# Kernel tuning notes

Measured on AMD Instinct MI355X. Metric: run time of the kernel, lower is better.

Reference implementation:

```python
import jax, jax.numpy as jnp
import numpy as np

N, G, D, H, B = 32768, 1024, 512, 768, 4   # nodes, graphs, hidden, shared, branches
GHD, NHD = 64, 3                           # graph head dim, node head dim (var_output=1)

def setup_inputs() -> dict:
    key = jax.random.key(0)
    ks = jax.random.split(key, 8)
    scale = 0.02
    x = jax.random.normal(ks[0], (N, D), dtype=jnp.float32)
    batch = jnp.sort(jax.random.randint(ks[1], (N,), 0, G, dtype=jnp.int32))
    dataset_name = jax.random.randint(ks[2], (G,), 0, B, dtype=jnp.int32)
    return {
        "x": x,
        "batch": batch,
        "dataset_name": dataset_name,
        "Wg_shared": jax.random.normal(ks[3], (B, D, H), jnp.float32) * scale,
        "bg_shared": jnp.zeros((B, H), jnp.float32),
        "Wg_head": jax.random.normal(ks[4], (B, H, 2 * GHD), jnp.float32) * scale,
        "bg_head": jnp.zeros((B, 2 * GHD), jnp.float32),
        "Wn1": jax.random.normal(ks[5], (B, D, D), jnp.float32) * scale,
        "bn1": jnp.zeros((B, D), jnp.float32),
        "Wn2": jax.random.normal(ks[6], (B, D, 2 * NHD), jnp.float32) * scale,
        "bn2": jnp.zeros((B, 2 * NHD), jnp.float32),
    }

def _select_branch(y, branch_ids):
    # y: [n, B, f], branch_ids: [n] -> [n, f]
    return jnp.take_along_axis(y, branch_ids[:, None, None], axis=1)[:, 0]

def reference(x, batch, dataset_name, Wg_shared, bg_shared, Wg_head, bg_head,
              Wn1, bn1, Wn2, bn2):
    nG = dataset_name.shape[0]
    # --- graph mean pooling (graph_pool_fn with reduction='mean') ---
    counts = jax.ops.segment_sum(jnp.ones((x.shape[0], 1), x.dtype), batch,
                                 num_segments=nG)
    x_graph = jax.ops.segment_sum(x, batch, num_segments=nG) / jnp.maximum(counts, 1.0)
    # --- graph head: per-dataset-ID branch dispatch (dense-MoE form) ---
    hg = jax.nn.relu(jnp.einsum('gd,bdh->gbh', x_graph, Wg_shared) + bg_shared)  # [G,B,H]
    hg_sel = _select_branch(hg, dataset_name)                                    # [G,H]
    og = jnp.einsum('gh,bho->gbo', hg_sel, Wg_head) + bg_head                    # [G,B,2*GHD]
    og_sel = _select_branch(og, dataset_name)
    graph_head = og_sel[:, :GHD]
    graph_var = og_sel[:, GHD:] ** 2
    # --- node head: route nodes by their graph's dataset ID (repeat_interleave) ---
    node_branch = dataset_name[batch]                                            # [N]
    hn = jax.nn.relu(jnp.einsum('nd,bdh->nbh', x, Wn1) + bn1)                    # [N,B,D]
    hn_sel = _select_branch(hn, node_branch)                                     # [N,D]
    on = jnp.einsum('nh,bho->nbo', hn_sel, Wn2) + bn2                            # [N,B,2*NHD]
    on_sel = _select_branch(on, node_branch)
    node_head = on_sel[:, :NHD]
    node_var = on_sel[:, NHD:] ** 2
    # torch returns (outputs, outputs_var); flattened here as 4 arrays
    return (graph_head, node_head, graph_var, node_var)
```

## Files before the change

### kernel.cpp

```cpp
#include <hip/hip_runtime.h>

#define N_NODES 32768
#define G_GRAPHS 1024
#define D_DIM 512
#define H_DIM 768
#define B_BR 4
#define GHD 64
#define NHD 3

#define NH_OFF (G_GRAPHS * GHD)
#define GV_OFF (G_GRAPHS * GHD + N_NODES * NHD)
#define NV_OFF (2 * G_GRAPHS * GHD + N_NODES * NHD)

typedef unsigned short ushort_t;
typedef __attribute__((ext_vector_type(8))) short short8;
typedef __attribute__((ext_vector_type(4))) float f32x4;
typedef __attribute__((ext_vector_type(4))) ushort_t ushort4_t;

__device__ __forceinline__ ushort_t rne_bf16(float v) {
  unsigned bits = __float_as_uint(v);
  return (ushort_t)((bits + 0x7fffu + ((bits >> 16) & 1u)) >> 16);
}

__global__ __launch_bounds__(1024) void segscan_kernel(
    const int* __restrict__ batch, const int* __restrict__ dsname,
    int* __restrict__ gstart, int* __restrict__ goff, int* __restrict__ glist,
    int* __restrict__ cnt, int* __restrict__ gcnt, int* __restrict__ pbase) {
  __shared__ int sg[G_GRAPHS + 1];
  __shared__ int scnt[4], sgcnt[4];
  const int tid = threadIdx.x;
  {
    int g = tid;
    int lo = 0, hi = N_NODES;
    while (lo < hi) { int mid = (lo + hi) >> 1; if (batch[mid] < g) lo = mid + 1; else hi = mid; }
    sg[g] = lo; gstart[g] = lo;
    if (tid == 0) { sg[G_GRAPHS] = N_NODES; gstart[G_GRAPHS] = N_NODES; }
  }
  __syncthreads();
  if (tid < 256) {
    const int lane = tid & 63;
    const int b = tid >> 6;
    int run_n = 0, run_g = 0;
    for (int c = 0; c < G_GRAPHS / 64; ++c) {
      int g = c * 64 + lane;
      int mine = (dsname[g] == b) ? 1 : 0;
      int len = mine ? (sg[g + 1] - sg[g]) : 0;
      int sl = len, so = mine;
#pragma unroll
      for (int off = 1; off < 64; off <<= 1) {
        int tl = __shfl_up(sl, off);
        int to = __shfl_up(so, off);
        if (lane >= off) { sl += tl; so += to; }
      }
      if (mine) {
        goff[g] = run_n + sl - len;
        glist[b * G_GRAPHS + run_g + so - 1] = g;
      }
      run_n += __shfl(sl, 63);
      run_g += __shfl(so, 63);
    }
    if (lane == 0) { scnt[b] = run_n; sgcnt[b] = run_g; }
  }
  __syncthreads();
  if (tid == 0) {
    int p = 0;
    for (int b2 = 0; b2 < 4; ++b2) {
      cnt[b2] = scnt[b2];
      gcnt[b2] = sgcnt[b2];
      pbase[b2] = p;
      p += (scnt[b2] + 63) & ~63;
    }
  }
}

__global__ __launch_bounds__(256) void prep_kernel(
    const float* __restrict__ x, const int* __restrict__ batch,
    const int* __restrict__ dsname, const int* __restrict__ gstart,
    const int* __restrict__ goff, const int* __restrict__ pbase,
    int* __restrict__ lists, ushort_t* __restrict__ xp,
    ushort_t* __restrict__ xgb,
    const float* __restrict__ Wn1, ushort_t* __restrict__ WPh,
    const float* __restrict__ Wg1, ushort_t* __restrict__ WG1,
    const float* __restrict__ Wgh, ushort_t* __restrict__ WG2,
    const float* __restrict__ Wn2, ushort_t* __restrict__ W2T) {
  __shared__ float Ws[64][65];
  const int bid = blockIdx.x;
  const int tid = threadIdx.x;

  if (bid < 512) {
    const int rl = tid >> 6;
    const int cs = tid & 63;
    float* red = (float*)Ws;
#pragma unroll
    for (int gi = 0; gi < 2; ++gi) {
      int g = bid * 2 + gi;
      int start = gstart[g], end = gstart[g + 1];
      int len = end - start;
      int b = dsname[g];
      int og = goff[g];
      int off0 = pbase[b] + og;
      float s0 = 0.f, s1 = 0.f, s2 = 0.f, s3 = 0.f;
      float s4 = 0.f, s5 = 0.f, s6 = 0.f, s7 = 0.f;
      for (int i = rl; i < len; i += 4) {
        int n = start + i;
        const float* sp = x + (size_t)n * D_DIM + cs * 8;
        float4 v0 = *reinterpret_cast<const float4*>(sp);
        float4 v1 = *reinterpret_cast<const float4*>(sp + 4);
        s0 += v0.x; s1 += v0.y; s2 += v0.z; s3 += v0.w;
        s4 += v1.x; s5 += v1.y; s6 += v1.z; s7 += v1.w;
        short8 h;
        h[0] = (short)rne_bf16(v0.x); h[1] = (short)rne_bf16(v0.y);
        h[2] = (short)rne_bf16(v0.z); h[3] = (short)rne_bf16(v0.w);
        h[4] = (short)rne_bf16(v1.x); h[5] = (short)rne_bf16(v1.y);
        h[6] = (short)rne_bf16(v1.z); h[7] = (short)rne_bf16(v1.w);
        int ib = og + i;
        *reinterpret_cast<short8*>(xp + (size_t)(off0 + i) * 512 + (cs ^ (ib & 7)) * 8) = h;
        if (cs == 0) lists[b * N_NODES + ib] = n;
      }
      float* rr = red + (rl * 64 + cs) * 8;
      rr[0] = s0; rr[1] = s1; rr[2] = s2; rr[3] = s3;
      rr[4] = s4; rr[5] = s5; rr[6] = s6; rr[7] = s7;
      __syncthreads();
      if (rl == 0) {
        float inv = (len > 0) ? 1.0f / (float)len : 0.0f;
        short8 h;
#pragma unroll
        for (int k = 0; k < 8; ++k) {
          float tot = red[(0 * 64 + cs) * 8 + k] + red[(1 * 64 + cs) * 8 + k] +
                      red[(2 * 64 + cs) * 8 + k] + red[(3 * 64 + cs) * 8 + k];
          h[k] = (short)rne_bf16(tot * inv);
        }
        *reinterpret_cast<short8*>(xgb + (size_t)g * D_DIM + cs * 8) = h;
      }
      __syncthreads();
    }
  } else {
    const int cid = bid - 512;
    if (cid < 256) {
      int b = cid >> 6, t = cid & 63;
      int kt = t >> 3, nt = t & 7;
      const float* W = Wn1 + (size_t)b * D_DIM * D_DIM;
      for (int i = tid; i < 64 * 64; i += 256) {
        int k = i >> 6, n = i & 63;
        Ws[k][n] = W[(size_t)(kt * 64 + k) * D_DIM + nt * 64 + n];
      }
      __syncthreads();
      for (int i = tid; i < 64 * 8; i += 256) {
        int n = i >> 3, kq8 = i & 7;
        short8 sh;
#pragma unroll
        for (int j = 0; j < 8; ++j) sh[j] = (short)rne_bf16(Ws[kq8 * 8 + j][n]);
        int gn = nt * 64 + n, gk0 = kt * 64 + kq8 * 8;
        int n16 = gn >> 4, l15 = gn & 15;
        int ks = gk0 >> 5, lq = (gk0 >> 3) & 3;
        size_t off = ((((size_t)b * 32 + n16) * 16 + ks) * 64 + lq * 16 + l15) * 8;
        *reinterpret_cast<short8*>(WPh + off) = sh;
      }
    } else if (cid < 640) {
      int l2 = cid - 256;
      int b = l2 / 96, t = l2 % 96;
      int kt = t / 12, nt = t % 12;
      const float* W = Wg1 + (size_t)b * D_DIM * H_DIM;
      for (int i = tid; i < 64 * 64; i += 256) {
        int k = i >> 6, n = i & 63;
        Ws[k][n] = W[(size_t)(kt * 64 + k) * H_DIM + nt * 64 + n];
      }
      __syncthreads();
      for (int i = tid; i < 64 * 8; i += 256) {
        int n = i >> 3, kq8 = i & 7;
        short8 sh;
#pragma unroll
        for (int j = 0; j < 8; ++j) sh[j] = (short)rne_bf16(Ws[kq8 * 8 + j][n]);
        int gn = nt * 64 + n, gk0 = kt * 64 + kq8 * 8;
        int n16 = gn >> 4, l15 = gn & 15;
        int ks = gk0 >> 5, lq = (gk0 >> 3) & 3;
        size_t off = ((((size_t)b * 48 + n16) * 16 + ks) * 64 + lq * 16 + l15) * 8;
        *reinterpret_cast<short8*>(WG1 + off) = sh;
      }
    } else if (cid < 644) {
      int b = cid - 640;
      const float* W = Wgh + (size_t)b * H_DIM * 2 * GHD;
      for (int i = tid; i < 8 * 24 * 64; i += 256) {
        int n16 = i / (24 * 64);
        int rem = i % (24 * 64);
        int ks = rem / 64, lane = rem % 64;
        int l15 = lane & 15, lq = lane >> 4;
        int o = n16 * 16 + l15;
        short8 sv;
#pragma unroll
        for (int j = 0; j < 8; ++j) {
          int k = ks * 32 + lq * 8 + j;
          sv[j] = (short)rne_bf16(W[(size_t)k * 128 + o]);
        }
        *reinterpret_cast<short8*>(WG2 + (size_t)i * 8 + (size_t)b * (8 * 24 * 64 * 8)) = sv;
      }
    } else {
      int b = cid - 644;
      for (int i = tid; i < 16 * D_DIM; i += 256) {
        int o = i & 15, c = i >> 4;
        float v = (o < 6) ? Wn2[(size_t)b * D_DIM * 6 + c * 6 + o] : 0.0f;
        W2T[(size_t)b * 16 * D_DIM + o * D_DIM + c] = rne_bf16(v);
      }
    }
  }
}

#define NBM 64
#define GRAPH_BLOCKS 128
#define NODE_BLOCKS 576

__global__ __launch_bounds__(512, 2) void mega_kernel(
    const ushort_t* __restrict__ xpacked,
    const ushort_t* __restrict__ WPh,
    const float* __restrict__ bn1,
    const ushort_t* __restrict__ W2T, const float* __restrict__ bn2,
    const int* __restrict__ cnt, const int* __restrict__ pbase,
    const int* __restrict__ lists,
    const ushort_t* __restrict__ xgb,
    const ushort_t* __restrict__ WG1, const float* __restrict__ bg_shared,
    const ushort_t* __restrict__ WG2, const float* __restrict__ bg_head,
    const int* __restrict__ gcnt, const int* __restrict__ glist,
    float* __restrict__ out) {
  __shared__ __align__(16) char smem[131072];
  __shared__ int idxbuf[64];

  const int bid = blockIdx.x;
  const int tid = threadIdx.x;
  const int lane = tid & 63;
  const int w = tid >> 6;
  const int l15 = lane & 15;
  const int lq = lane >> 4;

  if (bid >= GRAPH_BLOCKS) {
    const int nb = bid - GRAPH_BLOCKS;
    const int b = (nb & 7) >> 1;
    const int tile = ((nb >> 3) << 1) | (nb & 1);
    const int count = cnt[b];
    const int base = tile * NBM;
    if (base >= count) return;
    const int tile_base = pbase[b] + base;

    ushort_t* Ah = (ushort_t*)smem;
    if (tid < NBM) {
      int r = base + tid;
      idxbuf[tid] = (r < count) ? lists[b * N_NODES + r] : lists[b * N_NODES];
    }

    const char* srow = (const char*)(xpacked + (size_t)tile_base * 512);
#pragma unroll
    for (int i = 0; i < 8; ++i) {
      int row = w * 8 + i;
      const void* gsrc = srow + (size_t)row * 1024 + (size_t)lane * 16;
      __builtin_amdgcn_global_load_lds(
          (const __attribute__((address_space(1))) void*)gsrc,
          (__attribute__((address_space(3))) void*)((char*)Ah + row * 1024),
          16, 0, 0);
    }
    __syncthreads();

    const ushort_t* __restrict__ wph =
        WPh + (((size_t)b * 32 + w * 4) * 16) * 512 + (size_t)lane * 8;
    ushort_t* Bl = (ushort_t*)(smem + 65536 + w * 8192);

#pragma unroll
    for (int ct = 0; ct < 4; ++ct) {
      __builtin_amdgcn_global_load_lds(
          (const __attribute__((address_space(1))) void*)(wph + (size_t)(ct * 16) * 512),
          (__attribute__((address_space(3))) void*)(Bl + ct * 512),
          16, 0, 0);
    }

    f32x4 acc[4][4];
#pragma unroll
    for (int i = 0; i < 4; ++i)
#pragma unroll
      for (int j = 0; j < 4; ++j) acc[i][j] = (f32x4){0.f, 0.f, 0.f, 0.f};

#pragma unroll
    for (int ks = 0; ks < 16; ++ks) {
      const int nks = (ks + 1) & 15;
      ushort_t* Bnx = Bl + ((ks + 1) & 1) * 2048;
#pragma unroll
      for (int ct = 0; ct < 4; ++ct) {
        __builtin_amdgcn_global_load_lds(
            (const __attribute__((address_space(1))) void*)(wph + (size_t)(ct * 16 + nks) * 512),
            (__attribute__((address_space(3))) void*)(Bnx + ct * 512),
            16, 0, 0);
      }
      asm volatile("s_waitcnt vmcnt(4)" ::: "memory");
      __builtin_amdgcn_sched_barrier(0);
      const ushort_t* Bc = Bl + (ks & 1) * 2048;
      short8 ah[4], bh[4];
#pragma unroll
      for (int rt = 0; rt < 4; ++rt) {
        int R = rt * 16 + l15;
        int byteoff = R * 1024 + ((ks * 64 + lq * 16) ^ ((R & 7) << 4));
        ah[rt] = *reinterpret_cast<const short8*>((const char*)Ah + byteoff);
      }
#pragma unroll
      for (int ct = 0; ct < 4; ++ct)
        bh[ct] = *reinterpret_cast<const short8*>(Bc + ct * 512 + lane * 8);
#pragma unroll
      for (int ct = 0; ct < 4; ++ct) {
#pragma unroll
        for (int rt = 0; rt < 4; ++rt) {
          acc[rt][ct] = __builtin_amdgcn_mfma_f32_16x16x32_bf16(ah[rt], bh[ct], acc[rt][ct], 0, 0, 0);
        }
      }
    }

    __syncthreads();
    ushort_t* hn = Ah;
#pragma unroll
    for (int ct = 0; ct < 4; ++ct) {
      int n = w * 64 + ct * 16 + l15;
      float bias = bn1[b * D_DIM + n];
#pragma unroll
      for (int rt = 0; rt < 4; ++rt) {
#pragma unroll
        for (int j = 0; j < 4; ++j) {
          int row = rt * 16 + lq * 4 + j;
          float v = fmaxf(acc[rt][ct][j] + bias, 0.0f);
          int byteoff = row * 1024 + ((n * 2) ^ ((row & 7) << 4));
          *reinterpret_cast<ushort_t*>((char*)hn + byteoff) = rne_bf16(v);
        }
      }
    }
    __syncthreads();

    if (w < 4) {
      f32x4 acc2 = (f32x4){0.f, 0.f, 0.f, 0.f};
      const ushort_t* __restrict__ w2 =
          W2T + (size_t)b * (16 * 512) + (size_t)l15 * 512 + lq * 8;
      const int R = w * 16 + l15;
#pragma unroll
      for (int ks = 0; ks < 16; ++ks) {
        int byteoff = R * 1024 + ((ks * 64 + lq * 16) ^ ((R & 7) << 4));
        short8 a2 = *reinterpret_cast<const short8*>((const char*)hn + byteoff);
        short8 b2 = *reinterpret_cast<const short8*>(w2 + ks * 32);
        acc2 = __builtin_amdgcn_mfma_f32_16x16x32_bf16(a2, b2, acc2, 0, 0, 0);
      }
      int o = l15;
      if (o < 6) {
        float bo = bn2[b * 6 + o];
#pragma unroll
        for (int j = 0; j < 4; ++j) {
          int r = w * 16 + lq * 4 + j;
          if (base + r < count) {
            int n = idxbuf[r];
            float v = acc2[j] + bo;
            if (o < NHD) out[NH_OFF + n * NHD + o] = v;
            else out[NV_OFF + n * NHD + (o - NHD)] = v * v;
          }
        }
      }
    }
  } else {
    const int gb = bid;
    const int b = (gb & 7) >> 1;
    const int tile = ((gb >> 3) << 1) | (gb & 1);
    const int gc = gcnt[b];
    const int base = tile * 32;
    if (base >= gc) return;

    ushort_t* Ag = (ushort_t*)smem;
    if (tid < 32) {
      int r = base + tid;
      idxbuf[tid] = (r < gc) ? glist[b * G_GRAPHS + r] : glist[b * G_GRAPHS];
    }
    __syncthreads();

#pragma unroll
    for (int it = 0; it < 4; ++it) {
      int u = it * 512 + tid;
      int r = u >> 6, cp = u & 63;
      const ushort_t* sp = xgb + (size_t)idxbuf[r] * D_DIM + cp * 8;
      short8 h = *reinterpret_cast<const short8*>(sp);
      int byteoff = r * 1024 + ((cp * 16) ^ ((r & 7) << 4));
      *reinterpret_cast<short8*>((char*)Ag + byteoff) = h;
    }
    __syncthreads();

    f32x4 acc[2][6];
#pragma unroll
    for (int i = 0; i < 2; ++i)
#pragma unroll
      for (int j = 0; j < 6; ++j) acc[i][j] = (f32x4){0.f, 0.f, 0.f, 0.f};

    const ushort_t* __restrict__ g1 =
        WG1 + (((size_t)b * 48 + w * 6) * 16) * 512 + (size_t)lane * 8;

    for (int ks = 0; ks < 16; ++ks) {
      short8 ah[2];
#pragma unroll
      for (int rt = 0; rt < 2; ++rt) {
        int R = rt * 16 + l15;
        int byteoff = R * 1024 + ((ks * 64 + lq * 16) ^ ((R & 7) << 4));
        ah[rt] = *reinterpret_cast<const short8*>((const char*)Ag + byteoff);
      }
#pragma unroll
      for (int ct = 0; ct < 6; ++ct) {
        short8 bh = *reinterpret_cast<const short8*>(g1 + (size_t)(ct * 16 + ks) * 512);
#pragma unroll
        for (int rt = 0; rt < 2; ++rt) {
          acc[rt][ct] = __builtin_amdgcn_mfma_f32_16x16x32_bf16(ah[rt], bh, acc[rt][ct], 0, 0, 0);
        }
      }
    }

    __syncthreads();
    ushort_t* hgs = (ushort_t*)smem;
#pragma unroll
    for (int ct = 0; ct < 6; ++ct) {
      int n = w * 96 + ct * 16 + l15;
      float bias = bg_shared[b * H_DIM + n];
#pragma unroll
      for (int rt = 0; rt < 2; ++rt) {
#pragma unroll
        for (int j = 0; j < 4; ++j) {
          int row = rt * 16 + lq * 4 + j;
          float v = fmaxf(acc[rt][ct][j] + bias, 0.0f);
          int byteoff = row * 1536 + ((n * 2) ^ ((row & 7) << 4));
          *reinterpret_cast<ushort_t*>((char*)hgs + byteoff) = rne_bf16(v);
        }
      }
    }
    __syncthreads();

    f32x4 acc2[2];
    acc2[0] = (f32x4){0.f, 0.f, 0.f, 0.f};
    acc2[1] = (f32x4){0.f, 0.f, 0.f, 0.f};
    const ushort_t* __restrict__ g2 =
        WG2 + ((size_t)(b * 8 + w) * 24 * 64 + lane) * 8;

    for (int ks = 0; ks < 24; ++ks) {
      short8 b2 = *reinterpret_cast<const short8*>(g2 + (size_t)ks * 512);
#pragma unroll
      for (int rt = 0; rt < 2; ++rt) {
        int R = rt * 16 + l15;
        int byteoff = R * 1536 + ((ks * 64 + lq * 16) ^ ((R & 7) << 4));
        short8 a2 = *reinterpret_cast<const short8*>((const char*)hgs + byteoff);
        acc2[rt] = __builtin_amdgcn_mfma_f32_16x16x32_bf16(a2, b2, acc2[rt], 0, 0, 0);
      }
    }

    int o = w * 16 + l15;
    float bo = bg_head[b * 2 * GHD + o];
#pragma unroll
    for (int rt = 0; rt < 2; ++rt) {
#pragma unroll
      for (int j = 0; j < 4; ++j) {
        int r = rt * 16 + lq * 4 + j;
        if (base + r < gc) {
          int g = idxbuf[r];
          float v = acc2[rt][j] + bo;
          if (o < GHD) out[g * GHD + o] = v;
          else out[GV_OFF + g * GHD + (o - GHD)] = v * v;
        }
      }
    }
  }
}

extern "C" void kernel_launch(void* const* d_in, const int* in_sizes, int n_in,
                              void* d_out, int out_size, void* d_ws, size_t ws_size,
                              hipStream_t stream) {
  const float* x         = (const float*)d_in[0];
  const int*   batch     = (const int*)d_in[1];
  const int*   dsname    = (const int*)d_in[2];
  const float* Wg_shared = (const float*)d_in[3];
  const float* bg_shared = (const float*)d_in[4];
  const float* Wg_head   = (const float*)d_in[5];
  const float* bg_head   = (const float*)d_in[6];
  const float* Wn1       = (const float*)d_in[7];
  const float* bn1       = (const float*)d_in[8];
  const float* Wn2       = (const float*)d_in[9];
  const float* bn2       = (const float*)d_in[10];
  float* out = (float*)d_out;

  int* ws_i   = (int*)d_ws;
  int* cnt    = ws_i;
  int* gcnt   = ws_i + 8;
  int* pbase  = ws_i + 12;
  int* gstart = ws_i + 16;
  int* goff   = ws_i + 1056;
  int* glist  = ws_i + 2080;
  int* lists  = ws_i + 6176;
  ushort_t* xgb  = (ushort_t*)(ws_i + 137248);
  ushort_t* WPh  = xgb + 524288;
  ushort_t* W2T  = WPh + 1048576;
  ushort_t* WG1  = W2T + 32768;
  ushort_t* WG2  = WG1 + 1572864;
  ushort_t* xpacked = WG2 + 393216;

  segscan_kernel<<<1, 1024, 0, stream>>>(batch, dsname, gstart, goff, glist,
                                         cnt, gcnt, pbase);
  prep_kernel<<<1160, 256, 0, stream>>>(x, batch, dsname, gstart, goff, pbase,
                                        lists, xpacked, xgb,
                                        Wn1, WPh, Wg_shared, WG1,
                                        Wg_head, WG2, Wn2, W2T);
  mega_kernel<<<GRAPH_BLOCKS + NODE_BLOCKS, 512, 0, stream>>>(
      xpacked, WPh, bn1, W2T, bn2, cnt, pbase, lists,
      xgb, WG1, bg_shared, WG2, bg_head, gcnt, glist, out);
}
```

Before: 87.79 us.

## Widen prep parallelism, vectorize weight loads, reorder mega blocks and LDS waits

Result: slower. 94.10 us (+7.2%).

```diff
diff --git a/kernel.cpp b/kernel.cpp
--- a/kernel.cpp
+++ b/kernel.cpp
@@ -87,62 +87,71 @@
   const int bid = blockIdx.x;
   const int tid = threadIdx.x;
 
-  if (bid < 512) {
+  if (bid < 1024) {
     const int rl = tid >> 6;
     const int cs = tid & 63;
+    const int g = bid;
+    const int start = gstart[g];
+    const int len = gstart[g + 1] - start;
+    const int b = dsname[g];
+    const int og = goff[g];
+    const size_t off0 = (size_t)pbase[b] + og;
+    float s[8] = {0.f, 0.f, 0.f, 0.f, 0.f, 0.f, 0.f, 0.f};
+    for (int i0 = rl * 4; i0 < len; i0 += 16) {
+      float4 va[4], vb[4];
+#pragma unroll
+      for (int u = 0; u < 4; ++u) {
+        int i = i0 + u;
+        if (i < len) {
+          const float* sp = x + (size_t)(start + i) * D_DIM + cs * 8;
+          va[u] = *reinterpret_cast<const float4*>(sp);
+          vb[u] = *reinterpret_cast<const float4*>(sp + 4);
+        }
+      }
+#pragma unroll
+      for (int u = 0; u < 4; ++u) {
+        int i = i0 + u;
+        if (i < len) {
+          s[0] += va[u].x; s[1] += va[u].y; s[2] += va[u].z; s[3] += va[u].w;
+          s[4] += vb[u].x; s[5] += vb[u].y; s[6] += vb[u].z; s[7] += vb[u].w;
+          short8 h;
+          h[0] = (short)rne_bf16(va[u].x); h[1] = (short)rne_bf16(va[u].y);
+          h[2] = (short)rne_bf16(va[u].z); h[3] = (short)rne_bf16(va[u].w);
+          h[4] = (short)rne_bf16(vb[u].x); h[5] = (short)rne_bf16(vb[u].y);
+          h[6] = (short)rne_bf16(vb[u].z); h[7] = (short)rne_bf16(vb[u].w);
+          int ib = og + i;
+          *reinterpret_cast<short8*>(xp + (off0 + i) * 512 + (cs ^ (ib & 7)) * 8) = h;
+          if (cs == 0) lists[b * N_NODES + ib] = start + i;
+        }
+      }
+    }
     float* red = (float*)Ws;
-#pragma unroll
-    for (int gi = 0; gi < 2; ++gi) {
-      int g = bid * 2 + gi;
-      int start = gstart[g], end = gstart[g + 1];
-      int len = end - start;
-      int b = dsname[g];
-      int og = goff[g];
-      int off0 = pbase[b] + og;
-      float s0 = 0.f, s1 = 0.f, s2 = 0.f, s3 = 0.f;
-      float s4 = 0.f, s5 = 0.f, s6 = 0.f, s7 = 0.f;
-      for (int i = rl; i < len; i += 4) {
-        int n = start + i;
-        const float* sp = x + (size_t)n * D_DIM + cs * 8;
-        float4 v0 = *reinterpret_cast<const float4*>(sp);
-        float4 v1 = *reinterpret_cast<const float4*>(sp + 4);
-        s0 += v0.x; s1 += v0.y; s2 += v0.z; s3 += v0.w;
-        s4 += v1.x; s5 += v1.y; s6 += v1.z; s7 += v1.w;
-        short8 h;
-        h[0] = (short)rne_bf16(v0.x); h[1] = (short)rne_bf16(v0.y);
-        h[2] = (short)rne_bf16(v0.z); h[3] = (short)rne_bf16(v0.w);
-        h[4] = (short)rne_bf16(v1.x); h[5] = (short)rne_bf16(v1.y);
-        h[6] = (short)rne_bf16(v1.z); h[7] = (short)rne_bf16(v1.w);
-        int ib = og + i;
-        *reinterpret_cast<short8*>(xp + (size_t)(off0 + i) * 512 + (cs ^ (ib & 7)) * 8) = h;
-        if (cs == 0) lists[b * N_NODES + ib] = n;
-      }
-      float* rr = red + (rl * 64 + cs) * 8;
-      rr[0] = s0; rr[1] = s1; rr[2] = s2; rr[3] = s3;
-      rr[4] = s4; rr[5] = s5; rr[6] = s6; rr[7] = s7;
-      __syncthreads();
-      if (rl == 0) {
-        float inv = (len > 0) ? 1.0f / (float)len : 0.0f;
-        short8 h;
-#pragma unroll
-        for (int k = 0; k < 8; ++k) {
-          float tot = red[(0 * 64 + cs) * 8 + k] + red[(1 * 64 + cs) * 8 + k] +
-                      red[(2 * 64 + cs) * 8 + k] + red[(3 * 64 + cs) * 8 + k];
-          h[k] = (short)rne_bf16(tot * inv);
-        }
-        *reinterpret_cast<short8*>(xgb + (size_t)g * D_DIM + cs * 8) = h;
-      }
-      __syncthreads();
+    float* rr = red + (rl * 64 + cs) * 8;
+#pragma unroll
+    for (int k = 0; k < 8; ++k) rr[k] = s[k];
+    __syncthreads();
+    if (rl == 0) {
+      float inv = (len > 0) ? 1.0f / (float)len : 0.0f;
+      short8 h;
+#pragma unroll
+      for (int k = 0; k < 8; ++k) {
+        float tot = red[(0 * 64 + cs) * 8 + k] + red[(1 * 64 + cs) * 8 + k] +
+                    red[(2 * 64 + cs) * 8 + k] + red[(3 * 64 + cs) * 8 + k];
+        h[k] = (short)rne_bf16(tot * inv);
+      }
+      *reinterpret_cast<short8*>(xgb + (size_t)g * D_DIM + cs * 8) = h;
     }
   } else {
-    const int cid = bid - 512;
+    const int cid = bid - 1024;
     if (cid < 256) {
       int b = cid >> 6, t = cid & 63;
       int kt = t >> 3, nt = t & 7;
       const float* W = Wn1 + (size_t)b * D_DIM * D_DIM;
-      for (int i = tid; i < 64 * 64; i += 256) {
-        int k = i >> 6, n = i & 63;
-        Ws[k][n] = W[(size_t)(kt * 64 + k) * D_DIM + nt * 64 + n];
+      for (int i = tid; i < 64 * 16; i += 256) {
+        int k = i >> 4, n4 = (i & 15) << 2;
+        float4 v = *reinterpret_cast<const float4*>(
+            &W[(size_t)(kt * 64 + k) * D_DIM + nt * 64 + n4]);
+        Ws[k][n4] = v.x; Ws[k][n4 + 1] = v.y; Ws[k][n4 + 2] = v.z; Ws[k][n4 + 3] = v.w;
       }
       __syncthreads();
       for (int i = tid; i < 64 * 8; i += 256) {
@@ -161,9 +170,11 @@
       int b = l2 / 96, t = l2 % 96;
       int kt = t / 12, nt = t % 12;
       const float* W = Wg1 + (size_t)b * D_DIM * H_DIM;
-      for (int i = tid; i < 64 * 64; i += 256) {
-        int k = i >> 6, n = i & 63;
-        Ws[k][n] = W[(size_t)(kt * 64 + k) * H_DIM + nt * 64 + n];
+      for (int i = tid; i < 64 * 16; i += 256) {
+        int k = i >> 4, n4 = (i & 15) << 2;
+        float4 v = *reinterpret_cast<const float4*>(
+            &W[(size_t)(kt * 64 + k) * H_DIM + nt * 64 + n4]);
+        Ws[k][n4] = v.x; Ws[k][n4 + 1] = v.y; Ws[k][n4 + 2] = v.z; Ws[k][n4 + 3] = v.w;
       }
       __syncthreads();
       for (int i = tid; i < 64 * 8; i += 256) {
@@ -206,8 +217,8 @@
 }
 
 #define NBM 64
+#define NODE_BLOCKS 576
 #define GRAPH_BLOCKS 128
-#define NODE_BLOCKS 576
 
 __global__ __launch_bounds__(512, 2) void mega_kernel(
     const ushort_t* __restrict__ xpacked,
@@ -231,8 +242,8 @@
   const int l15 = lane & 15;
   const int lq = lane >> 4;
 
-  if (bid >= GRAPH_BLOCKS) {
-    const int nb = bid - GRAPH_BLOCKS;
+  if (bid < NODE_BLOCKS) {
+    const int nb = bid;
     const int b = (nb & 7) >> 1;
     const int tile = ((nb >> 3) << 1) | (nb & 1);
     const int count = cnt[b];
@@ -287,16 +298,17 @@
             (__attribute__((address_space(3))) void*)(Bnx + ct * 512),
             16, 0, 0);
       }
-      asm volatile("s_waitcnt vmcnt(4)" ::: "memory");
-      __builtin_amdgcn_sched_barrier(0);
-      const ushort_t* Bc = Bl + (ks & 1) * 2048;
-      short8 ah[4], bh[4];
+      short8 ah[4];
 #pragma unroll
       for (int rt = 0; rt < 4; ++rt) {
         int R = rt * 16 + l15;
         int byteoff = R * 1024 + ((ks * 64 + lq * 16) ^ ((R & 7) << 4));
         ah[rt] = *reinterpret_cast<const short8*>((const char*)Ah + byteoff);
       }
+      asm volatile("s_waitcnt vmcnt(4)" ::: "memory");
+      __builtin_amdgcn_sched_barrier(0);
+      const ushort_t* Bc = Bl + (ks & 1) * 2048;
+      short8 bh[4];
 #pragma unroll
       for (int ct = 0; ct < 4; ++ct)
         bh[ct] = *reinterpret_cast<const short8*>(Bc + ct * 512 + lane * 8);
@@ -356,7 +368,7 @@
       }
     }
   } else {
-    const int gb = bid;
+    const int gb = bid - NODE_BLOCKS;
     const int b = (gb & 7) >> 1;
     const int tile = ((gb >> 3) << 1) | (gb & 1);
     const int gc = gcnt[b];
@@ -495,11 +507,11 @@
 
   segscan_kernel<<<1, 1024, 0, stream>>>(batch, dsname, gstart, goff, glist,
                                          cnt, gcnt, pbase);
-  prep_kernel<<<1160, 256, 0, stream>>>(x, batch, dsname, gstart, goff, pbase,
+  prep_kernel<<<1672, 256, 0, stream>>>(x, batch, dsname, gstart, goff, pbase,
                                         lists, xpacked, xgb,
                                         Wn1, WPh, Wg_shared, WG1,
                                         Wg_head, WG2, Wn2, W2T);
-  mega_kernel<<<GRAPH_BLOCKS + NODE_BLOCKS, 512, 0, stream>>>(
+  mega_kernel<<<NODE_BLOCKS + GRAPH_BLOCKS, 512, 0, stream>>>(
       xpacked, WPh, bn1, W2T, bn2, cnt, pbase, lists,
       xgb, WG1, bg_shared, WG2, bg_head, gcnt, glist, out);
 }
```
